# Kernel optimization log

Hardware: AMD Instinct MI355X
Metric: run time of the kernel (lower is better)

The kernel has to match this reference:

```python
import jax, jax.numpy as jnp
import numpy as np

D_FEATURE = 1024
HEAD = 16
D_K = 64
D_V = 64
EPS = 1e-6


def setup_inputs() -> dict:
    key = jax.random.key(0)
    ks = jax.random.split(key, 12)
    B, S = 2, 2048
    s_in = 1.0 / np.sqrt(D_FEATURE)
    s_o = 1.0 / np.sqrt(HEAD * D_V)
    return {
        "q": jax.random.normal(ks[0], (B, S, D_FEATURE), jnp.float32),
        "k": jax.random.normal(ks[1], (B, S, D_FEATURE), jnp.float32),
        "v": jax.random.normal(ks[2], (B, S, D_FEATURE), jnp.float32),
        "Wq": jax.random.uniform(ks[3], (D_FEATURE, HEAD * D_K), jnp.float32, -s_in, s_in),
        "bq": jnp.zeros((HEAD * D_K,), jnp.float32),
        "Wk": jax.random.uniform(ks[4], (D_FEATURE, HEAD * D_K), jnp.float32, -s_in, s_in),
        "bk": jnp.zeros((HEAD * D_K,), jnp.float32),
        "Wv": jax.random.uniform(ks[5], (D_FEATURE, HEAD * D_V), jnp.float32, -s_in, s_in),
        "bv": jnp.zeros((HEAD * D_V,), jnp.float32),
        "Wo": jax.random.uniform(ks[6], (HEAD * D_V, D_FEATURE), jnp.float32, -s_o, s_o),
        "bo": jnp.zeros((D_FEATURE,), jnp.float32),
        "gamma": jnp.ones((D_FEATURE,), jnp.float32),
        "beta": jnp.zeros((D_FEATURE,), jnp.float32),
    }


def reference(q, k, v, Wq, bq, Wk, bk, Wv, bv, Wo, bo, gamma, beta):
    B, Sq, _ = q.shape
    Sk, Sv = k.shape[1], v.shape[1]
    shortcut = v
    # projections -> (b, h, s, d)
    qh = (q @ Wq + bq).reshape(B, Sq, HEAD, D_K).transpose(0, 2, 1, 3)
    kh = (k @ Wk + bk).reshape(B, Sk, HEAD, D_K).transpose(0, 2, 1, 3)
    vh = (v @ Wv + bv).reshape(B, Sv, HEAD, D_V).transpose(0, 2, 1, 3)
    scale = 1.0 / np.sqrt(D_K).astype(np.float32)
    scores = jnp.einsum('bhqd,bhkd->bhqk', qh * scale, kh)
    attn = jax.nn.softmax(scores, axis=-1)  # dropout is identity (p=0 / eval)
    ctx = jnp.einsum('bhqk,bhkd->bhqd', attn, vh)
    ctx = ctx.transpose(0, 2, 1, 3).reshape(B, Sv, HEAD * D_V)
    out = ctx @ Wo + bo
    out = out + shortcut
    # LayerNorm, eps=1e-6
    mu = out.mean(-1, keepdims=True)
    var = out.var(-1, keepdims=True)
    out = (out - mu) * jax.lax.rsqrt(var + EPS) * gamma + beta
    return out
```

## Files before the change

kernel.cpp:

```cpp
#include <hip/hip_runtime.h>

#define D_FEAT 1024
#define NTOK   4096
#define SEQ    2048
#define NHEAD  16
#define DK     64
#define QSCALE 0.1803368801111204f

typedef float          f32x4  __attribute__((ext_vector_type(4)));
typedef float          f32x16 __attribute__((ext_vector_type(16)));
typedef short          s16x8  __attribute__((ext_vector_type(8)));
typedef unsigned short u16x4  __attribute__((ext_vector_type(4)));

__device__ __forceinline__ unsigned short f2bf(float f) {
  union { float f; unsigned int u; } x; x.f = f;
  unsigned int r = x.u + 0x7fffu + ((x.u >> 16) & 1u);
  return (unsigned short)(r >> 16);
}
__device__ __forceinline__ unsigned short f2h(float f) {
  union { _Float16 h; unsigned short u; } x; x.h = (_Float16)f; return x.u;
}
__device__ __forceinline__ float h2f(unsigned short u) {
  union { _Float16 h; unsigned short u; } x; x.u = u; return (float)x.h;
}

__device__ __forceinline__ f32x4 mfma16(s16x8 a, s16x8 b, f32x4 c) {
  return __builtin_amdgcn_mfma_f32_16x16x32_bf16(a, b, c, 0, 0, 0);
}
__device__ __forceinline__ f32x16 mfma32(s16x8 a, s16x8 b, f32x16 c) {
  return __builtin_amdgcn_mfma_f32_32x32x16_bf16(a, b, c, 0, 0, 0);
}

__device__ __forceinline__ void gload16(const void* g, void* l) {
  __builtin_amdgcn_global_load_lds(
      (const __attribute__((address_space(1))) void*)g,
      (__attribute__((address_space(3))) void*)l, 16, 0, 0);
}

__global__ __launch_bounds__(256) void prep_kernel(
    const float* __restrict__ q, const float* __restrict__ k, const float* __restrict__ v,
    const float* __restrict__ Wq, const float* __restrict__ Wk,
    const float* __restrict__ Wv, const float* __restrict__ Wo,
    unsigned short* __restrict__ qb, unsigned short* __restrict__ kb,
    unsigned short* __restrict__ vb,
    unsigned short* __restrict__ WT, unsigned short* __restrict__ Wot)
{
  __shared__ float tile[32][33];
  const int bx = blockIdx.x, tid = threadIdx.x;
  if (bx < 12288) {
    int sel = bx >> 12;
    const float* src = sel == 0 ? q : (sel == 1 ? k : v);
    unsigned short* dst = sel == 0 ? qb : (sel == 1 ? kb : vb);
    size_t i = ((size_t)(bx & 4095) * 256 + tid) * 4;
    float4 f = *(const float4*)(src + i);
    u16x4 o; o.x = f2bf(f.x); o.y = f2bf(f.y); o.z = f2bf(f.z); o.w = f2bf(f.w);
    *(u16x4*)(dst + i) = o;
  } else {
    int t = bx - 12288;
    int z = t >> 10, rest = t & 1023;
    int bxt = rest & 31, byt = rest >> 5;
    const float* W = z == 0 ? Wq : z == 1 ? Wk : z == 2 ? Wv : Wo;
    unsigned short* T = (z < 3) ? (WT + (size_t)z * 1024 * 1024) : Wot;
    int tx = tid & 31, ty = tid >> 5;
    int n = bxt * 32 + tx;
    for (int i = 0; i < 4; ++i) {
      int kk = byt * 32 + ty + i * 8;
      tile[ty + i * 8][tx] = W[(size_t)kk * D_FEAT + n];
    }
    __syncthreads();
    int kk = byt * 32 + tx;
    for (int i = 0; i < 4; ++i) {
      int n2 = bxt * 32 + ty + i * 8;
      T[(size_t)n2 * D_FEAT + kk] = f2bf(tile[tx][ty + i * 8]);
    }
  }
}

__global__ __launch_bounds__(256, 3) void gemm_qkv(
    const unsigned short* __restrict__ qb, const unsigned short* __restrict__ kb,
    const unsigned short* __restrict__ vb, const unsigned short* __restrict__ WT,
    const float* __restrict__ bq, const float* __restrict__ bk, const float* __restrict__ bv,
    unsigned short* __restrict__ Qp, unsigned short* __restrict__ Kp, unsigned short* __restrict__ Vt)
{
  __shared__ __align__(16) unsigned short sAB[2 * 128 * 64];
  unsigned short* sA = sAB;
  unsigned short* sB = sAB + 128 * 64;
  const int tid = threadIdx.x;
  const int wave = tid >> 6, lane = tid & 63;
  const int quad = lane >> 4, l16 = lane & 15;
  const int wx = wave & 1, wy = wave >> 1;
  const int bx = blockIdx.x;
  const int chunk = bx >> 3;

  const unsigned short* rA;
  const unsigned short* rB;
  int m0, n0;
  if (chunk < 2) {
    m0 = blockIdx.y * 128; n0 = (bx & 7) * 128;
    rA = (chunk ? kb : qb) + (size_t)m0 * D_FEAT;
    rB = WT + (size_t)(chunk * 1024 + n0) * D_FEAT;
  } else {
    m0 = (bx & 7) * 128; n0 = blockIdx.y * 128;
    rA = WT + (size_t)(2048 + m0) * D_FEAT;
    rB = vb + (size_t)n0 * D_FEAT;
  }

  f32x4 acc[4][4];
  for (int mt = 0; mt < 4; ++mt)
    for (int nt = 0; nt < 4; ++nt) acc[mt][nt] = (f32x4){0.f, 0.f, 0.f, 0.f};

  const int rw8 = lane >> 3;
  const int cls = ((lane & 7) ^ (lane >> 3)) * 8;
  const int sw = l16 & 7;

  for (int k0 = 0; k0 < D_FEAT; k0 += 64) {
    __syncthreads();
    for (int j = 0; j < 4; ++j) {
      int ch = wave * 4 + j;
      gload16(rA + (size_t)(ch * 8 + rw8) * D_FEAT + k0 + cls, sA + ch * 512);
      gload16(rB + (size_t)(ch * 8 + rw8) * D_FEAT + k0 + cls, sB + ch * 512);
    }
    __syncthreads();
    s16x8 af[2][4], bfr[2][4];
    for (int kk = 0; kk < 2; ++kk) {
      int c = ((kk * 4 + quad) ^ sw) * 8;
      for (int mt = 0; mt < 4; ++mt)
        af[kk][mt] = *(const s16x8*)(sA + (wy * 64 + mt * 16 + l16) * 64 + c);
      for (int nt = 0; nt < 4; ++nt)
        bfr[kk][nt] = *(const s16x8*)(sB + (wx * 64 + nt * 16 + l16) * 64 + c);
    }
    for (int kk = 0; kk < 2; ++kk)
      for (int mt = 0; mt < 4; ++mt)
        for (int nt = 0; nt < 4; ++nt)
          acc[mt][nt] = mfma16(af[kk][mt], bfr[kk][nt], acc[mt][nt]);
  }

  if (chunk < 2) {
    const float* bias = chunk ? bk : bq;
    unsigned short* Cp = chunk ? Kp : Qp;
    const float scale = chunk == 0 ? QSCALE : 1.0f;
    for (int mt = 0; mt < 4; ++mt)
      for (int nt = 0; nt < 4; ++nt) {
        int col = n0 + wx * 64 + nt * 16 + l16;
        float bcol = bias[col];
        for (int r = 0; r < 4; ++r) {
          int row = m0 + wy * 64 + mt * 16 + quad * 4 + r;
          Cp[(size_t)row * D_FEAT + col] = f2bf((acc[mt][nt][r] + bcol) * scale);
        }
      }
  } else {
    for (int mt = 0; mt < 4; ++mt)
      for (int r = 0; r < 4; ++r) {
        float bfeat = bv[m0 + wy * 64 + mt * 16 + quad * 4 + r];
        for (int nt = 0; nt < 4; ++nt) acc[mt][nt][r] += bfeat;
      }
    unsigned short* tb = sAB;
    for (int p = 0; p < 2; ++p) {
      __syncthreads();
      if (wx == p) {
        for (int mt = 0; mt < 4; ++mt)
          for (int nt = 0; nt < 4; ++nt) {
            int tok_loc = nt * 16 + l16;
            for (int r = 0; r < 4; ++r) {
              int f_loc = wy * 64 + mt * 16 + quad * 4 + r;
              tb[f_loc * 72 + tok_loc] = f2bf(acc[mt][nt][r]);
            }
          }
      }
      __syncthreads();
      int n_base = n0 + p * 64;
      int b = n_base >> 11, tok0 = n_base & 2047;
      int ck = lane & 7;
      for (int j = 0; j < 4; ++j) {
        int f_loc = (wave * 4 + j) * 8 + rw8;
        int f = m0 + f_loc, hh = f >> 6, dv = f & 63;
        *(s16x8*)(Vt + ((size_t)(b * 16 + hh) * 64 + dv) * SEQ + tok0 + ck * 8) =
            *(const s16x8*)(tb + f_loc * 72 + ck * 8);
      }
    }
  }
}

__global__ __launch_bounds__(256) void gemm_o(
    const unsigned short* __restrict__ A, const unsigned short* __restrict__ Bt,
    const float* __restrict__ bias, const float* __restrict__ resid,
    float* __restrict__ Cout)
{
  __shared__ __align__(16) unsigned short sA[128 * 64];
  __shared__ __align__(16) unsigned short sB[64 * 64];
  const int tid = threadIdx.x;
  const int wave = tid >> 6, lane = tid & 63;
  const int quad = lane >> 4, l16 = lane & 15;
  const int wx = wave & 1, wy = wave >> 1;
  const int n0 = blockIdx.x * 64, m0 = blockIdx.y * 128;

  f32x4 acc[4][2];
  for (int mt = 0; mt < 4; ++mt)
    for (int nt = 0; nt < 2; ++nt) acc[mt][nt] = (f32x4){0.f, 0.f, 0.f, 0.f};

  const int rw8 = lane >> 3;
  const int cls = ((lane & 7) ^ (lane >> 3)) * 8;
  const int sw = l16 & 7;

  for (int k0 = 0; k0 < D_FEAT; k0 += 64) {
    __syncthreads();
    for (int j = 0; j < 4; ++j) {
      int ch = wave * 4 + j;
      gload16(A + (size_t)(m0 + ch * 8 + rw8) * D_FEAT + k0 + cls, sA + ch * 512);
    }
    for (int j = 0; j < 2; ++j) {
      int ch = wave * 2 + j;
      gload16(Bt + (size_t)(n0 + ch * 8 + rw8) * D_FEAT + k0 + cls, sB + ch * 512);
    }
    __syncthreads();
    s16x8 af[2][4], bfr[2][2];
    for (int kk = 0; kk < 2; ++kk) {
      int c = ((kk * 4 + quad) ^ sw) * 8;
      for (int mt = 0; mt < 4; ++mt)
        af[kk][mt] = *(const s16x8*)(sA + (wy * 64 + mt * 16 + l16) * 64 + c);
      for (int nt = 0; nt < 2; ++nt)
        bfr[kk][nt] = *(const s16x8*)(sB + (wx * 32 + nt * 16 + l16) * 64 + c);
    }
    for (int kk = 0; kk < 2; ++kk)
      for (int mt = 0; mt < 4; ++mt)
        for (int nt = 0; nt < 2; ++nt)
          acc[mt][nt] = mfma16(af[kk][mt], bfr[kk][nt], acc[mt][nt]);
  }

  for (int mt = 0; mt < 4; ++mt)
    for (int nt = 0; nt < 2; ++nt) {
      int col = n0 + wx * 32 + nt * 16 + l16;
      float bcol = bias[col];
      for (int r = 0; r < 4; ++r) {
        int row = m0 + wy * 64 + mt * 16 + quad * 4 + r;
        Cout[(size_t)row * D_FEAT + col] =
            acc[mt][nt][r] + bcol + resid[(size_t)row * D_FEAT + col];
      }
    }
}

__global__ __launch_bounds__(256, 4) void flash_part(
    const unsigned short* __restrict__ Qp,
    const unsigned short* __restrict__ Kp,
    const unsigned short* __restrict__ Vt,
    unsigned short* __restrict__ Opart,
    float* __restrict__ L)
{
  __shared__ __align__(16) unsigned short sQ[128 * 64];
  __shared__ __align__(16) unsigned short sK[64 * 64];
  __shared__ __align__(16) unsigned short sV[64 * 64];

  const int tid = threadIdx.x;
  const int wave = tid >> 6, lane = tid & 63;
  const int l32 = lane & 31, h = lane >> 5;

  const int blk = blockIdx.x;
  const int xcd = blk & 7, jj = blk >> 3;
  const int grp = xcd * 8 + (jj >> 4);
  const int q0 = (jj & 15) * 128;
  const int bh = grp & 31, z = grp >> 5;
  const int b = bh >> 4, hd = bh & 15;
  const int kbase = z * (SEQ / 2);
  const size_t base = (size_t)b * SEQ * D_FEAT + (size_t)hd * DK;
  const unsigned short* vt = Vt + (size_t)bh * 64 * SEQ;

  const int rw8 = lane >> 3;
  const int cls = ((lane & 7) ^ (lane >> 3)) * 8;

  for (int j = 0; j < 4; ++j) {
    int ch = wave * 4 + j;
    gload16(Qp + base + (size_t)(q0 + ch * 8 + rw8) * D_FEAT + cls, sQ + ch * 512);
  }
  __syncthreads();

  const int qrow = wave * 32 + l32;
  const int qsw = qrow & 7;
  s16x8 bq[4];
  for (int s = 0; s < 4; ++s)
    bq[s] = *(const s16x8*)(sQ + qrow * 64 + ((2 * s + h) ^ qsw) * 8);

  unsigned short* sP = sQ;

  f32x16 o0, o1;
  for (int r = 0; r < 16; ++r) { o0[r] = 0.f; o1[r] = 0.f; }
  float lsum = 0.f;

  const int ksw0 = l32 & 7;

  for (int k0 = kbase; k0 < kbase + SEQ / 2; k0 += 64) {
    __syncthreads();
    for (int j = 0; j < 2; ++j) {
      int ch = wave * 2 + j;
      gload16(Kp + base + (size_t)(k0 + ch * 8 + rw8) * D_FEAT + cls, sK + ch * 512);
      gload16(vt + (size_t)(ch * 8 + rw8) * SEQ + k0 + cls, sV + ch * 512);
    }
    __syncthreads();

    f32x16 st0, st1;
    for (int r = 0; r < 16; ++r) { st0[r] = 0.f; st1[r] = 0.f; }
    for (int s = 0; s < 4; ++s) {
      int csw = ((2 * s + h) ^ ksw0) * 8;
      s16x8 a0 = *(const s16x8*)(sK + l32 * 64 + csw);
      s16x8 a1 = *(const s16x8*)(sK + (32 + l32) * 64 + csw);
      st0 = mfma32(a0, bq[s], st0);
      st1 = mfma32(a1, bq[s], st1);
    }

    const int rowb = qrow * 64;
    for (int g = 0; g < 4; ++g) {
      unsigned int u[4];
      for (int r = 0; r < 4; ++r) {
        union { float f; unsigned int v; } x;
        x.f = __builtin_exp2f(st0[4 * g + r]);
        lsum += x.f; u[r] = x.v;
      }
      unsigned int w0 = __builtin_amdgcn_perm(u[1], u[0], 0x07060302u);
      unsigned int w1 = __builtin_amdgcn_perm(u[3], u[2], 0x07060302u);
      *(uint2*)(sP + rowb + ((g ^ qsw) * 8) + 4 * h) = make_uint2(w0, w1);
    }
    for (int g = 0; g < 4; ++g) {
      unsigned int u[4];
      for (int r = 0; r < 4; ++r) {
        union { float f; unsigned int v; } x;
        x.f = __builtin_exp2f(st1[4 * g + r]);
        lsum += x.f; u[r] = x.v;
      }
      unsigned int w0 = __builtin_amdgcn_perm(u[1], u[0], 0x07060302u);
      unsigned int w1 = __builtin_amdgcn_perm(u[3], u[2], 0x07060302u);
      *(uint2*)(sP + rowb + (((4 + g) ^ qsw) * 8) + 4 * h) = make_uint2(w0, w1);
    }

    s16x8 bp[4];
    for (int s = 0; s < 4; ++s)
      bp[s] = *(const s16x8*)(sP + rowb + ((2 * s + h) ^ qsw) * 8);

    for (int s = 0; s < 4; ++s) {
      int csw = ((2 * s + h) ^ ksw0) * 8;
      s16x8 a0 = *(const s16x8*)(sV + l32 * 64 + csw);
      s16x8 a1 = *(const s16x8*)(sV + (32 + l32) * 64 + csw);
      o0 = mfma32(a0, bp[s], o0);
      o1 = mfma32(a1, bp[s], o1);
    }
  }

  lsum += __shfl_xor(lsum, 32, 64);
  const size_t trow = (size_t)(z * 32 + bh) * SEQ + (q0 + qrow);
  unsigned short* orow = Opart + trow * 64;
  for (int g = 0; g < 4; ++g) {
    u16x4 ov;
    for (int r = 0; r < 4; ++r) ov[r] = f2h(o0[4 * g + r]);
    *(u16x4*)(orow + 8 * g + 4 * h) = ov;
  }
  for (int g = 0; g < 4; ++g) {
    u16x4 ov;
    for (int r = 0; r < 4; ++r) ov[r] = f2h(o1[4 * g + r]);
    *(u16x4*)(orow + 32 + 8 * g + 4 * h) = ov;
  }
  if (h == 0) L[trow] = lsum;
}

__global__ __launch_bounds__(256) void combine_kernel(
    const unsigned short* __restrict__ Opart, const float* __restrict__ L,
    unsigned short* __restrict__ ctx)
{
  const int idx = blockIdx.x * 256 + threadIdx.x;
  const int dq = idx & 15;
  const int trow = idx >> 4;
  const int bh = trow >> 11, tok = trow & 2047;
  const int b = bh >> 4, h = bh & 15;
  const int HS = 32 * SEQ;

  float inv = __builtin_amdgcn_rcpf(L[trow] + L[HS + trow]);

  u16x4 p0 = *(const u16x4*)(Opart + (size_t)trow * 64 + dq * 4);
  u16x4 p1 = *(const u16x4*)(Opart + ((size_t)HS + trow) * 64 + dq * 4);
  u16x4 o;
  for (int r = 0; r < 4; ++r)
    o[r] = f2bf((h2f(p0[r]) + h2f(p1[r])) * inv);
  *(u16x4*)(ctx + (size_t)b * SEQ * D_FEAT + (size_t)tok * D_FEAT + h * 64 + dq * 4) = o;
}

__global__ __launch_bounds__(256) void ln_kernel(
    const float* __restrict__ x, const float* __restrict__ gamma,
    const float* __restrict__ beta, float* __restrict__ out)
{
  const int row = blockIdx.x, tid = threadIdx.x;
  const int wave = tid >> 6, lane = tid & 63;
  const float* xr = x + (size_t)row * D_FEAT;
  float4 v = ((const float4*)xr)[tid];
  float s  = v.x + v.y + v.z + v.w;
  float ss = v.x * v.x + v.y * v.y + v.z * v.z + v.w * v.w;
  for (int off = 1; off < 64; off <<= 1) {
    s  += __shfl_xor(s,  off, 64);
    ss += __shfl_xor(ss, off, 64);
  }
  __shared__ float red[8];
  if (lane == 0) { red[wave] = s; red[wave + 4] = ss; }
  __syncthreads();
  s  = red[0] + red[1] + red[2] + red[3];
  ss = red[4] + red[5] + red[6] + red[7];
  float mean = s * (1.f / D_FEAT);
  float var  = ss * (1.f / D_FEAT) - mean * mean;
  float rstd = rsqrtf(var + 1e-6f);
  float4 g  = ((const float4*)gamma)[tid];
  float4 bt = ((const float4*)beta)[tid];
  float4 o;
  o.x = (v.x - mean) * rstd * g.x + bt.x;
  o.y = (v.y - mean) * rstd * g.y + bt.y;
  o.z = (v.z - mean) * rstd * g.z + bt.z;
  o.w = (v.w - mean) * rstd * g.w + bt.w;
  ((float4*)(out + (size_t)row * D_FEAT))[tid] = o;
}

extern "C" void kernel_launch(void* const* d_in, const int* in_sizes, int n_in,
                              void* d_out, int out_size, void* d_ws, size_t ws_size,
                              hipStream_t stream) {
  const float* q     = (const float*)d_in[0];
  const float* k     = (const float*)d_in[1];
  const float* v     = (const float*)d_in[2];
  const float* Wq    = (const float*)d_in[3];
  const float* bq    = (const float*)d_in[4];
  const float* Wk    = (const float*)d_in[5];
  const float* bk    = (const float*)d_in[6];
  const float* Wv    = (const float*)d_in[7];
  const float* bv    = (const float*)d_in[8];
  const float* Wo    = (const float*)d_in[9];
  const float* bo    = (const float*)d_in[10];
  const float* gamma = (const float*)d_in[11];
  const float* beta  = (const float*)d_in[12];

  char* w = (char*)d_ws;
  const size_t MB = 1u << 20;
  unsigned short* qb    = (unsigned short*)(w + 0 * MB);
  unsigned short* kb    = (unsigned short*)(w + 8 * MB);
  unsigned short* vb    = (unsigned short*)(w + 16 * MB);
  unsigned short* WT    = (unsigned short*)(w + 24 * MB);
  unsigned short* Wot   = (unsigned short*)(w + 30 * MB);
  unsigned short* Qp    = (unsigned short*)(w + 32 * MB);
  unsigned short* Kp    = (unsigned short*)(w + 40 * MB);
  unsigned short* Vt    = (unsigned short*)(w + 48 * MB);
  unsigned short* ctx   = (unsigned short*)(w + 56 * MB);
  float*          tmp   = (float*)(w + 64 * MB);
  unsigned short* Opart = (unsigned short*)(w + 0 * MB);
  float*          L     = (float*)(w + 16 * MB);

  prep_kernel<<<16384, 256, 0, stream>>>(q, k, v, Wq, Wk, Wv, Wo, qb, kb, vb, WT, Wot);

  gemm_qkv<<<dim3(24, 32), 256, 0, stream>>>(qb, kb, vb, WT, bq, bk, bv, Qp, Kp, Vt);

  flash_part<<<1024, 256, 0, stream>>>(Qp, Kp, Vt, Opart, L);

  combine_kernel<<<4096, 256, 0, stream>>>(Opart, L, ctx);

  gemm_o<<<dim3(16, 32), 256, 0, stream>>>(ctx, Wot, bo, v, tmp);

  ln_kernel<<<NTOK, 256, 0, stream>>>(tmp, gamma, beta, (float*)d_out);
}
```

Measured before the change: 246.4 us.

## Double-buffer K/V tiles and pass P through registers in flash attention

The flash attention kernel now double-buffers K/V tiles in shared memory, so the next tile's global-to-LDS load is issued before the current tile is computed, and the loop needs one barrier per iteration instead of two. The P matrix no longer round-trips through LDS. It is packed to bf16 with v_cvt_pk_bf16_f32 and rearranged across lanes with v_permlane32_swap into MFMA operands. MFMA sections are wrapped in s_setprio. The cost is double the K/V LDS footprint, and correctness depends on the permlane layout matching the operand layout the previous LDS path produced.

```diff
diff --git a/kernel.cpp b/kernel.cpp
--- a/kernel.cpp
+++ b/kernel.cpp
@@ -35,6 +35,20 @@
   __builtin_amdgcn_global_load_lds(
       (const __attribute__((address_space(1))) void*)g,
       (__attribute__((address_space(3))) void*)l, 16, 0, 0);
+}
+
+__device__ __forceinline__ unsigned int cvtpk(float a, float b) {
+  unsigned int r;
+  asm("v_cvt_pk_bf16_f32 %0, %1, %2" : "=v"(r) : "v"(a), "v"(b));
+  return r;
+}
+__device__ __forceinline__ void swap32(unsigned int& x, unsigned int& y) {
+  asm("v_permlane32_swap_b32 %0, %1" : "+v"(x), "+v"(y));
+}
+__device__ __forceinline__ s16x8 mk8(unsigned int a, unsigned int b,
+                                     unsigned int c, unsigned int d) {
+  union { unsigned int u[4]; s16x8 v; } x;
+  x.u[0] = a; x.u[1] = b; x.u[2] = c; x.u[3] = d; return x.v;
 }
 
 __global__ __launch_bounds__(256) void prep_kernel(
@@ -246,9 +260,7 @@
     unsigned short* __restrict__ Opart,
     float* __restrict__ L)
 {
-  __shared__ __align__(16) unsigned short sQ[128 * 64];
-  __shared__ __align__(16) unsigned short sK[64 * 64];
-  __shared__ __align__(16) unsigned short sV[64 * 64];
+  __shared__ __align__(16) unsigned short sKV[2][8192];
 
   const int tid = threadIdx.x;
   const int wave = tid >> 6, lane = tid & 63;
@@ -269,88 +281,113 @@
 
   for (int j = 0; j < 4; ++j) {
     int ch = wave * 4 + j;
-    gload16(Qp + base + (size_t)(q0 + ch * 8 + rw8) * D_FEAT + cls, sQ + ch * 512);
+    gload16(Qp + base + (size_t)(q0 + ch * 8 + rw8) * D_FEAT + cls, &sKV[1][ch * 512]);
   }
   __syncthreads();
+
+  for (int j = 0; j < 2; ++j) {
+    int ch = wave * 2 + j;
+    gload16(Kp + base + (size_t)(kbase + ch * 8 + rw8) * D_FEAT + cls, &sKV[0][ch * 512]);
+    gload16(vt + (size_t)(ch * 8 + rw8) * SEQ + kbase + cls, &sKV[0][4096 + ch * 512]);
+  }
 
   const int qrow = wave * 32 + l32;
   const int qsw = qrow & 7;
   s16x8 bq[4];
+#pragma unroll
   for (int s = 0; s < 4; ++s)
-    bq[s] = *(const s16x8*)(sQ + qrow * 64 + ((2 * s + h) ^ qsw) * 8);
-
-  unsigned short* sP = sQ;
+    bq[s] = *(const s16x8*)(&sKV[1][qrow * 64 + ((2 * s + h) ^ qsw) * 8]);
+  __syncthreads();
 
   f32x16 o0, o1;
+#pragma unroll
   for (int r = 0; r < 16; ++r) { o0[r] = 0.f; o1[r] = 0.f; }
   float lsum = 0.f;
 
   const int ksw0 = l32 & 7;
-
-  for (int k0 = kbase; k0 < kbase + SEQ / 2; k0 += 64) {
-    __syncthreads();
-    for (int j = 0; j < 2; ++j) {
-      int ch = wave * 2 + j;
-      gload16(Kp + base + (size_t)(k0 + ch * 8 + rw8) * D_FEAT + cls, sK + ch * 512);
-      gload16(vt + (size_t)(ch * 8 + rw8) * SEQ + k0 + cls, sV + ch * 512);
-    }
-    __syncthreads();
+  const int NT = (SEQ / 2) / 64;
+
+  int cur = 0;
+  for (int t = 0; t < NT; ++t) {
+    if (t + 1 < NT) {
+      int k1 = kbase + (t + 1) * 64;
+      unsigned short* dst = sKV[cur ^ 1];
+      for (int j = 0; j < 2; ++j) {
+        int ch = wave * 2 + j;
+        gload16(Kp + base + (size_t)(k1 + ch * 8 + rw8) * D_FEAT + cls, dst + ch * 512);
+        gload16(vt + (size_t)(ch * 8 + rw8) * SEQ + k1 + cls, dst + 4096 + ch * 512);
+      }
+    }
+
+    const unsigned short* bK = sKV[cur];
+    const unsigned short* bV = sKV[cur] + 4096;
 
     f32x16 st0, st1;
+#pragma unroll
     for (int r = 0; r < 16; ++r) { st0[r] = 0.f; st1[r] = 0.f; }
+
+    __builtin_amdgcn_s_setprio(1);
+#pragma unroll
     for (int s = 0; s < 4; ++s) {
       int csw = ((2 * s + h) ^ ksw0) * 8;
-      s16x8 a0 = *(const s16x8*)(sK + l32 * 64 + csw);
-      s16x8 a1 = *(const s16x8*)(sK + (32 + l32) * 64 + csw);
+      s16x8 a0 = *(const s16x8*)(bK + l32 * 64 + csw);
+      s16x8 a1 = *(const s16x8*)(bK + (32 + l32) * 64 + csw);
       st0 = mfma32(a0, bq[s], st0);
       st1 = mfma32(a1, bq[s], st1);
     }
-
-    const int rowb = qrow * 64;
-    for (int g = 0; g < 4; ++g) {
-      unsigned int u[4];
-      for (int r = 0; r < 4; ++r) {
-        union { float f; unsigned int v; } x;
-        x.f = __builtin_exp2f(st0[4 * g + r]);
-        lsum += x.f; u[r] = x.v;
-      }
-      unsigned int w0 = __builtin_amdgcn_perm(u[1], u[0], 0x07060302u);
-      unsigned int w1 = __builtin_amdgcn_perm(u[3], u[2], 0x07060302u);
-      *(uint2*)(sP + rowb + ((g ^ qsw) * 8) + 4 * h) = make_uint2(w0, w1);
-    }
-    for (int g = 0; g < 4; ++g) {
-      unsigned int u[4];
-      for (int r = 0; r < 4; ++r) {
-        union { float f; unsigned int v; } x;
-        x.f = __builtin_exp2f(st1[4 * g + r]);
-        lsum += x.f; u[r] = x.v;
-      }
-      unsigned int w0 = __builtin_amdgcn_perm(u[1], u[0], 0x07060302u);
-      unsigned int w1 = __builtin_amdgcn_perm(u[3], u[2], 0x07060302u);
-      *(uint2*)(sP + rowb + (((4 + g) ^ qsw) * 8) + 4 * h) = make_uint2(w0, w1);
-    }
+    __builtin_amdgcn_s_setprio(0);
+
+    float ex0[16], ex1[16];
+#pragma unroll
+    for (int r = 0; r < 16; ++r) {
+      ex0[r] = __builtin_exp2f(st0[r]);
+      ex1[r] = __builtin_exp2f(st1[r]);
+    }
+#pragma unroll
+    for (int r = 0; r < 16; ++r) lsum += ex0[r] + ex1[r];
+
+    unsigned int c0[8], c1[8];
+#pragma unroll
+    for (int i = 0; i < 8; ++i) {
+      c0[i] = cvtpk(ex0[2 * i], ex0[2 * i + 1]);
+      c1[i] = cvtpk(ex1[2 * i], ex1[2 * i + 1]);
+    }
+    swap32(c0[0], c0[2]); swap32(c0[1], c0[3]);
+    swap32(c0[4], c0[6]); swap32(c0[5], c0[7]);
+    swap32(c1[0], c1[2]); swap32(c1[1], c1[3]);
+    swap32(c1[4], c1[6]); swap32(c1[5], c1[7]);
 
     s16x8 bp[4];
-    for (int s = 0; s < 4; ++s)
-      bp[s] = *(const s16x8*)(sP + rowb + ((2 * s + h) ^ qsw) * 8);
-
+    bp[0] = mk8(c0[0], c0[1], c0[2], c0[3]);
+    bp[1] = mk8(c0[4], c0[5], c0[6], c0[7]);
+    bp[2] = mk8(c1[0], c1[1], c1[2], c1[3]);
+    bp[3] = mk8(c1[4], c1[5], c1[6], c1[7]);
+
+    __builtin_amdgcn_s_setprio(1);
+#pragma unroll
     for (int s = 0; s < 4; ++s) {
       int csw = ((2 * s + h) ^ ksw0) * 8;
-      s16x8 a0 = *(const s16x8*)(sV + l32 * 64 + csw);
-      s16x8 a1 = *(const s16x8*)(sV + (32 + l32) * 64 + csw);
+      s16x8 a0 = *(const s16x8*)(bV + l32 * 64 + csw);
+      s16x8 a1 = *(const s16x8*)(bV + (32 + l32) * 64 + csw);
       o0 = mfma32(a0, bp[s], o0);
       o1 = mfma32(a1, bp[s], o1);
     }
+    __builtin_amdgcn_s_setprio(0);
+
+    if (t + 1 < NT) __syncthreads();
+    cur ^= 1;
   }
 
   lsum += __shfl_xor(lsum, 32, 64);
   const size_t trow = (size_t)(z * 32 + bh) * SEQ + (q0 + qrow);
   unsigned short* orow = Opart + trow * 64;
+#pragma unroll
   for (int g = 0; g < 4; ++g) {
     u16x4 ov;
     for (int r = 0; r < 4; ++r) ov[r] = f2h(o0[4 * g + r]);
     *(u16x4*)(orow + 8 * g + 4 * h) = ov;
   }
+#pragma unroll
   for (int g = 0; g < 4; ++g) {
     u16x4 ov;
     for (int r = 0; r < 4; ++r) ov[r] = f2h(o1[4 * g + r]);
```

New measurement: 248.4 us. About the same (+0.8%).

## Triple-buffer flash K/V tiles and keep P in registers via permlane swap

Applied to the files above, without the earlier changes.

Rewrites the flash attention inner loop to use 32-key tiles staged through a three-slot LDS ring, so global-to-LDS loads for tile t+2 overlap compute on tile t with a single barrier per step. Q fragments are loaded straight from global into registers. The softmax probabilities are packed with v_cvt_pk_bf16_f32 and rearranged with v_permlane32_swap, which removes the LDS round-trip for P. It also adds s_setprio around MFMA groups. This trades more hand-scheduled inline asm and specific vmcnt accounting for fewer barriers and less LDS traffic, and the rounding now goes through the hardware bf16 convert rather than truncation.

```diff
diff --git a/kernel.cpp b/kernel.cpp
--- a/kernel.cpp
+++ b/kernel.cpp
@@ -35,6 +35,24 @@
   __builtin_amdgcn_global_load_lds(
       (const __attribute__((address_space(1))) void*)g,
       (__attribute__((address_space(3))) void*)l, 16, 0, 0);
+}
+
+__device__ __forceinline__ float fexp2(float x) {
+  return __builtin_amdgcn_exp2f(x);
+}
+
+__device__ __forceinline__ unsigned int cvtpk(float a, float b) {
+  unsigned int r;
+  asm("v_cvt_pk_bf16_f32 %0, %1, %2" : "=v"(r) : "v"(a), "v"(b));
+  return r;
+}
+__device__ __forceinline__ void swap32(unsigned int& x, unsigned int& y) {
+  asm("v_permlane32_swap_b32 %0, %1" : "+v"(x), "+v"(y));
+}
+__device__ __forceinline__ s16x8 mk8(unsigned int a, unsigned int b,
+                                     unsigned int c, unsigned int d) {
+  union { unsigned int u[4]; s16x8 v; } x;
+  x.u[0] = a; x.u[1] = b; x.u[2] = c; x.u[3] = d; return x.v;
 }
 
 __global__ __launch_bounds__(256) void prep_kernel(
@@ -246,9 +264,7 @@
     unsigned short* __restrict__ Opart,
     float* __restrict__ L)
 {
-  __shared__ __align__(16) unsigned short sQ[128 * 64];
-  __shared__ __align__(16) unsigned short sK[64 * 64];
-  __shared__ __align__(16) unsigned short sV[64 * 64];
+  __shared__ __align__(16) unsigned short sB3[3][4096];
 
   const int tid = threadIdx.x;
   const int wave = tid >> 6, lane = tid & 63;
@@ -264,93 +280,111 @@
   const size_t base = (size_t)b * SEQ * D_FEAT + (size_t)hd * DK;
   const unsigned short* vt = Vt + (size_t)bh * 64 * SEQ;
 
-  const int rw8 = lane >> 3;
-  const int cls = ((lane & 7) ^ (lane >> 3)) * 8;
-
-  for (int j = 0; j < 4; ++j) {
-    int ch = wave * 4 + j;
-    gload16(Qp + base + (size_t)(q0 + ch * 8 + rw8) * D_FEAT + cls, sQ + ch * 512);
-  }
-  __syncthreads();
-
   const int qrow = wave * 32 + l32;
-  const int qsw = qrow & 7;
+
+  const unsigned short* qptr = Qp + base + (size_t)(q0 + qrow) * D_FEAT;
   s16x8 bq[4];
+#pragma unroll
   for (int s = 0; s < 4; ++s)
-    bq[s] = *(const s16x8*)(sQ + qrow * 64 + ((2 * s + h) ^ qsw) * 8);
-
-  unsigned short* sP = sQ;
+    bq[s] = *(const s16x8*)(qptr + (2 * s + h) * 8);
+
+  const int krow = tid >> 3;
+  const unsigned short* kPtr =
+      Kp + base + (size_t)(kbase + krow) * D_FEAT + (((tid & 7) ^ (krow & 7)) * 8);
+  const int vrow = tid >> 2;
+  const unsigned short* vPtr =
+      vt + (size_t)vrow * SEQ + kbase + (((tid & 3) ^ (vrow & 3)) * 8);
+
+  const int kdst = wave * 512;
+  gload16(kPtr, &sB3[0][kdst]);
+  gload16(vPtr, &sB3[0][2048 + kdst]);
+  kPtr += 32 * D_FEAT; vPtr += 32;
+  gload16(kPtr, &sB3[1][kdst]);
+  gload16(vPtr, &sB3[1][2048 + kdst]);
+  kPtr += 32 * D_FEAT; vPtr += 32;
 
   f32x16 o0, o1;
+#pragma unroll
   for (int r = 0; r < 16; ++r) { o0[r] = 0.f; o1[r] = 0.f; }
-  float lsum = 0.f;
-
-  const int ksw0 = l32 & 7;
-
-  for (int k0 = kbase; k0 < kbase + SEQ / 2; k0 += 64) {
-    __syncthreads();
-    for (int j = 0; j < 2; ++j) {
-      int ch = wave * 2 + j;
-      gload16(Kp + base + (size_t)(k0 + ch * 8 + rw8) * D_FEAT + cls, sK + ch * 512);
-      gload16(vt + (size_t)(ch * 8 + rw8) * SEQ + k0 + cls, sV + ch * 512);
-    }
-    __syncthreads();
-
-    f32x16 st0, st1;
-    for (int r = 0; r < 16; ++r) { st0[r] = 0.f; st1[r] = 0.f; }
-    for (int s = 0; s < 4; ++s) {
-      int csw = ((2 * s + h) ^ ksw0) * 8;
-      s16x8 a0 = *(const s16x8*)(sK + l32 * 64 + csw);
-      s16x8 a1 = *(const s16x8*)(sK + (32 + l32) * 64 + csw);
-      st0 = mfma32(a0, bq[s], st0);
-      st1 = mfma32(a1, bq[s], st1);
-    }
-
-    const int rowb = qrow * 64;
-    for (int g = 0; g < 4; ++g) {
-      unsigned int u[4];
-      for (int r = 0; r < 4; ++r) {
-        union { float f; unsigned int v; } x;
-        x.f = __builtin_exp2f(st0[4 * g + r]);
-        lsum += x.f; u[r] = x.v;
-      }
-      unsigned int w0 = __builtin_amdgcn_perm(u[1], u[0], 0x07060302u);
-      unsigned int w1 = __builtin_amdgcn_perm(u[3], u[2], 0x07060302u);
-      *(uint2*)(sP + rowb + ((g ^ qsw) * 8) + 4 * h) = make_uint2(w0, w1);
-    }
-    for (int g = 0; g < 4; ++g) {
-      unsigned int u[4];
-      for (int r = 0; r < 4; ++r) {
-        union { float f; unsigned int v; } x;
-        x.f = __builtin_exp2f(st1[4 * g + r]);
-        lsum += x.f; u[r] = x.v;
-      }
-      unsigned int w0 = __builtin_amdgcn_perm(u[1], u[0], 0x07060302u);
-      unsigned int w1 = __builtin_amdgcn_perm(u[3], u[2], 0x07060302u);
-      *(uint2*)(sP + rowb + (((4 + g) ^ qsw) * 8) + 4 * h) = make_uint2(w0, w1);
-    }
-
-    s16x8 bp[4];
-    for (int s = 0; s < 4; ++s)
-      bp[s] = *(const s16x8*)(sP + rowb + ((2 * s + h) ^ qsw) * 8);
-
-    for (int s = 0; s < 4; ++s) {
-      int csw = ((2 * s + h) ^ ksw0) * 8;
-      s16x8 a0 = *(const s16x8*)(sV + l32 * 64 + csw);
-      s16x8 a1 = *(const s16x8*)(sV + (32 + l32) * 64 + csw);
-      o0 = mfma32(a0, bp[s], o0);
-      o1 = mfma32(a1, bp[s], o1);
-    }
-  }
-
+  float lsA = 0.f, lsB = 0.f;
+
+  const int kxor = l32 & 7;
+  const int vxor = l32 & 3;
+  const int NT = (SEQ / 2) / 32;
+
+#define FLASH_TILE(BUF)                                                        \
+  {                                                                            \
+    const unsigned short* bK = &sB3[BUF][0];                                   \
+    const unsigned short* bV = &sB3[BUF][2048];                                \
+    f32x16 st;                                                                 \
+    _Pragma("unroll") for (int r = 0; r < 16; ++r) st[r] = 0.f;                \
+    __builtin_amdgcn_s_setprio(1);                                            \
+    _Pragma("unroll") for (int s = 0; s < 4; ++s) {                            \
+      s16x8 a = *(const s16x8*)(bK + l32 * 64 + (((2 * s + h) ^ kxor) * 8));   \
+      st = mfma32(a, bq[s], st);                                               \
+    }                                                                          \
+    __builtin_amdgcn_s_setprio(0);                                            \
+    unsigned int c[8];                                                         \
+    _Pragma("unroll") for (int i = 0; i < 8; ++i) {                            \
+      float e0 = fexp2(st[2 * i]);                                             \
+      float e1 = fexp2(st[2 * i + 1]);                                         \
+      lsA += e0; lsB += e1;                                                    \
+      c[i] = cvtpk(e0, e1);                                                    \
+    }                                                                          \
+    swap32(c[0], c[2]); swap32(c[1], c[3]);                                    \
+    swap32(c[4], c[6]); swap32(c[5], c[7]);                                    \
+    s16x8 bp0 = mk8(c[0], c[1], c[2], c[3]);                  \
+    s16x8 bp1 = mk8(c[4], c[5], c[6], c[7]);                  \
+    __builtin_amdgcn_s_setprio(1);                                            \
+    _Pragma("unroll") for (int kk = 0; kk < 2; ++kk) {                         \
+      int cs = ((2 * kk + h) ^ vxor) * 8;                                      \
+      s16x8 av0 = *(const s16x8*)(bV + l32 * 32 + cs);                         \
+      s16x8 av1 = *(const s16x8*)(bV + (32 + l32) * 32 + cs);                  \
+      s16x8 bp = kk ? bp1 : bp0;                                               \
+      o0 = mfma32(av0, bp, o0);                                                \
+      o1 = mfma32(av1, bp, o1);                                                \
+    }                                                                          \
+    __builtin_amdgcn_s_setprio(0);                                            \
+  }
+
+#define FLASH_STEP(CURB, NXT2B)                                                \
+  {                                                                            \
+    asm volatile("s_waitcnt vmcnt(2)" ::: "memory");                           \
+    __builtin_amdgcn_s_barrier();                                             \
+    __builtin_amdgcn_sched_barrier(0);                                        \
+    gload16(kPtr, &sB3[NXT2B][kdst]);                                          \
+    gload16(vPtr, &sB3[NXT2B][2048 + kdst]);                                   \
+    kPtr += 32 * D_FEAT; vPtr += 32;                                           \
+    FLASH_TILE(CURB);                                                          \
+  }
+
+  for (int t3 = 0; t3 < NT - 2; t3 += 3) {
+    FLASH_STEP(0, 2);
+    FLASH_STEP(1, 0);
+    FLASH_STEP(2, 1);
+  }
+  asm volatile("s_waitcnt vmcnt(2)" ::: "memory");
+  __builtin_amdgcn_s_barrier();
+  __builtin_amdgcn_sched_barrier(0);
+  FLASH_TILE(0);
+  asm volatile("s_waitcnt vmcnt(0)" ::: "memory");
+  __builtin_amdgcn_s_barrier();
+  __builtin_amdgcn_sched_barrier(0);
+  FLASH_TILE(1);
+#undef FLASH_STEP
+#undef FLASH_TILE
+
+  float lsum = lsA + lsB;
   lsum += __shfl_xor(lsum, 32, 64);
   const size_t trow = (size_t)(z * 32 + bh) * SEQ + (q0 + qrow);
   unsigned short* orow = Opart + trow * 64;
+#pragma unroll
   for (int g = 0; g < 4; ++g) {
     u16x4 ov;
     for (int r = 0; r < 4; ++r) ov[r] = f2h(o0[4 * g + r]);
     *(u16x4*)(orow + 8 * g + 4 * h) = ov;
   }
+#pragma unroll
   for (int g = 0; g < 4; ++g) {
     u16x4 ov;
     for (int r = 0; r < 4; ++r) ov[r] = f2h(o1[4 * g + r]);
```

New measurement: 232.9 us. -5.5%, faster.
